# Optimization experiments

Measured on AMD Instinct MI355X. Metric: run time of the kernel, lower is better.

## Reference

```python
import jax, jax.numpy as jnp
import numpy as np

B, C, H, W = 64, 1, 512, 512
THRESHOLD = 50.0
LEVELS = 3


def _haar_dwt2(x):
    """Single-level 2D Haar DWT on [B,H,W] (even H,W). Returns (cA,(cH,cV,cD)).
    Matches pywt 'haar' coefficient magnitudes (sign conventions are irrelevant
    to the loss, which is odd-symmetric through soft-threshold and uses |.|)."""
    a = x[:, 0::2, 0::2]
    b = x[:, 0::2, 1::2]
    c = x[:, 1::2, 0::2]
    d = x[:, 1::2, 1::2]
    half = jnp.float32(0.5)
    cA = (a + b + c + d) * half
    cH = (a + b - c - d) * half  # low along cols, high along rows
    cV = (a - b + c - d) * half  # high along cols, low along rows
    cD = (a - b - c + d) * half  # high/high
    return cA, (cH, cV, cD)


def _wavedec2(x, levels):
    """Multi-level DWT. Returns detail tuples ordered coarsest-first,
    matching pywt.wavedec2 list order coeffs[1:]."""
    details = []
    cA = x
    for _ in range(levels):
        cA, d = _haar_dwt2(cA)
        details.append(d)
    details.reverse()  # coarsest first
    return details


def _soft_threshold(x, thr):
    return jnp.sign(x) * jnp.maximum(jnp.abs(x) - thr, 0.0)


def setup_inputs() -> dict:
    key = jax.random.key(0)
    k1, k2 = jax.random.split(key)
    pred = jax.random.uniform(k1, (B, C, H, W), dtype=jnp.float32)
    target = jax.random.uniform(k2, (B, C, H, W), dtype=jnp.float32)
    return {"pred": pred, "target": target}


def reference(pred, target):
    p = pred[:, 0]   # [B,H,W]
    t = target[:, 0]
    det_p = _wavedec2(p, LEVELS)
    det_t = _wavedec2(t, LEVELS)
    total = jnp.float32(0.0)
    for level_idx in range(1, LEVELS + 1):
        # per-level adaptive threshold, normalized to [0,1] image range
        thr = jnp.float32((THRESHOLD / 2.0 ** (level_idx - 1)) / 255.0)
        level_weight = jnp.float32(1.0 / level_idx)
        dp = det_p[level_idx - 1]
        dt = det_t[level_idx - 1]
        level_loss = jnp.float32(0.0)
        for k in range(3):  # cH, cV, cD
            diff = _soft_threshold(dp[k], thr) - _soft_threshold(dt[k], thr)
            level_loss = level_loss + jnp.mean(jnp.abs(diff))
        total = total + level_weight * level_loss / 3.0
    # per-sample sum / valid_samples == batch mean (all samples valid here)
    return total
```

## Files before the change

kernel.cpp:

```cpp
#include <hip/hip_runtime.h>


#define IMG_H 512
#define IMG_W 512
#define N_BATCH 64

#define THR1 (50.0f / 255.0f)
#define THR2 (25.0f / 255.0f)
#define THR3 (12.5f / 255.0f)

#define GRID_BLOCKS 2048
#define N_ITERS 2

__device__ __forceinline__ float softthr(float x, float thr) {
    float m = fmaxf(fabsf(x) - thr, 0.0f);
    return copysignf(m, x);
}

__device__ __forceinline__ float detail_term(float p, float t, float thr) {
    return fabsf(softthr(p, thr) - softthr(t, thr));
}

__device__ __forceinline__ void haar_quad(float a, float b, float c, float d,
                                          float& cA, float& cH, float& cV, float& cD) {
    cA = 0.5f * (a + b + c + d);
    cH = 0.5f * (a + b - c - d);
    cV = 0.5f * (a - b + c - d);
    cD = 0.5f * (a - b - c + d);
}

__global__ __launch_bounds__(256, 8)
void wavelet_main(const float* __restrict__ pred,
                  const float* __restrict__ target,
                  float* __restrict__ ws) {
    constexpr float W1 = 1.0f / (1.0f * 3.0f * (float)(N_BATCH * 256 * 256));
    constexpr float W2 = 1.0f / (2.0f * 3.0f * (float)(N_BATCH * 128 * 128));
    constexpr float W3 = 1.0f / (3.0f * 3.0f * (float)(N_BATCH * 64 * 64));

    const int tid0 = blockIdx.x * 256 + threadIdx.x;
    float acc = 0.0f;

    #pragma unroll
    for (int iter = 0; iter < N_ITERS; ++iter) {
        const int it   = tid0 + iter * (GRID_BLOCKS * 256);
        const int lane = it & 63;
        const int wv   = it >> 6;
        const int img  = wv >> 8;
        const int ww   = wv & 255;
        const int wcy  = ww >> 2;
        const int wcx  = ww & 3;
        const int half = lane >> 5;
        const int li   = lane & 31;

        const int r0 = 8 * wcy + 4 * half;
        const int c0 = 128 * wcx + 4 * li;
        const long base = (long)img * (IMG_H * IMG_W) + (long)r0 * IMG_W + c0;

        const float4 p0 = *(const float4*)(pred + base);
        const float4 p1 = *(const float4*)(pred + base + IMG_W);
        const float4 p2 = *(const float4*)(pred + base + 2 * IMG_W);
        const float4 p3 = *(const float4*)(pred + base + 3 * IMG_W);
        const float4 t0 = *(const float4*)(target + base);
        const float4 t1 = *(const float4*)(target + base + IMG_W);
        const float4 t2 = *(const float4*)(target + base + 2 * IMG_W);
        const float4 t3 = *(const float4*)(target + base + 3 * IMG_W);

        float s1 = 0.0f;
        float cA1p[4], cA1t[4];
        {
            float cA, cH, cV, cD, cAt, cHt, cVt, cDt;
            haar_quad(p0.x, p0.y, p1.x, p1.y, cA, cH, cV, cD);
            haar_quad(t0.x, t0.y, t1.x, t1.y, cAt, cHt, cVt, cDt);
            s1 += detail_term(cH, cHt, THR1) + detail_term(cV, cVt, THR1) + detail_term(cD, cDt, THR1);
            cA1p[0] = cA; cA1t[0] = cAt;

            haar_quad(p0.z, p0.w, p1.z, p1.w, cA, cH, cV, cD);
            haar_quad(t0.z, t0.w, t1.z, t1.w, cAt, cHt, cVt, cDt);
            s1 += detail_term(cH, cHt, THR1) + detail_term(cV, cVt, THR1) + detail_term(cD, cDt, THR1);
            cA1p[1] = cA; cA1t[1] = cAt;

            haar_quad(p2.x, p2.y, p3.x, p3.y, cA, cH, cV, cD);
            haar_quad(t2.x, t2.y, t3.x, t3.y, cAt, cHt, cVt, cDt);
            s1 += detail_term(cH, cHt, THR1) + detail_term(cV, cVt, THR1) + detail_term(cD, cDt, THR1);
            cA1p[2] = cA; cA1t[2] = cAt;

            haar_quad(p2.z, p2.w, p3.z, p3.w, cA, cH, cV, cD);
            haar_quad(t2.z, t2.w, t3.z, t3.w, cAt, cHt, cVt, cDt);
            s1 += detail_term(cH, cHt, THR1) + detail_term(cV, cVt, THR1) + detail_term(cD, cDt, THR1);
            cA1p[3] = cA; cA1t[3] = cAt;
        }

        float s2 = 0.0f;
        float cA2p, cA2t;
        {
            float cH, cV, cD, cHt, cVt, cDt;
            haar_quad(cA1p[0], cA1p[1], cA1p[2], cA1p[3], cA2p, cH, cV, cD);
            haar_quad(cA1t[0], cA1t[1], cA1t[2], cA1t[3], cA2t, cHt, cVt, cDt);
            s2 = detail_term(cH, cHt, THR2) + detail_term(cV, cVt, THR2) + detail_term(cD, cDt, THR2);
        }

        float s3 = 0.0f;
        {
            float pV = __shfl_xor(cA2p, 32);
            float tV = __shfl_xor(cA2t, 32);
            float pH = __shfl_xor(cA2p, 1);
            float tH = __shfl_xor(cA2t, 1);
            float pD = __shfl_xor(pV, 1);
            float tD = __shfl_xor(tV, 1);
            float cA, cH, cV, cD, cAt, cHt, cVt, cDt;
            haar_quad(cA2p, pH, pV, pD, cA, cH, cV, cD);
            haar_quad(cA2t, tH, tV, tD, cAt, cHt, cVt, cDt);
            s3 = detail_term(cH, cHt, THR3) + detail_term(cV, cVt, THR3) + detail_term(cD, cDt, THR3);
        }
        const float w3 = ((lane & 33) == 0) ? W3 : 0.0f;

        acc += W1 * s1 + W2 * s2 + w3 * s3;
    }

    #pragma unroll
    for (int off = 32; off > 0; off >>= 1)
        acc += __shfl_down(acc, off, 64);

    __shared__ float wave_sums[4];
    const int lane_b = threadIdx.x & 63;
    const int wave_b = threadIdx.x >> 6;
    if (lane_b == 0) wave_sums[wave_b] = acc;
    __syncthreads();
    if (threadIdx.x == 0)
        ws[blockIdx.x] = wave_sums[0] + wave_sums[1] + wave_sums[2] + wave_sums[3];
}

__global__ __launch_bounds__(256)
void wavelet_reduce(const float* __restrict__ ws, float* __restrict__ out) {
    const int tidx = threadIdx.x;
    float v = 0.0f;
    #pragma unroll
    for (int k = 0; k < GRID_BLOCKS / 256; ++k)
        v += ws[tidx + k * 256];

    #pragma unroll
    for (int off = 32; off > 0; off >>= 1)
        v += __shfl_down(v, off, 64);

    __shared__ float wave_sums[4];
    const int lane = tidx & 63;
    const int wave = tidx >> 6;
    if (lane == 0) wave_sums[wave] = v;
    __syncthreads();
    if (tidx == 0)
        out[0] = wave_sums[0] + wave_sums[1] + wave_sums[2] + wave_sums[3];
}

extern "C" void kernel_launch(void* const* d_in, const int* in_sizes, int n_in,
                              void* d_out, int out_size, void* d_ws, size_t ws_size,
                              hipStream_t stream) {
    const float* pred   = (const float*)d_in[0];
    const float* target = (const float*)d_in[1];
    float* out = (float*)d_out;
    float* ws  = (float*)d_ws;

    wavelet_main<<<GRID_BLOCKS, 256, 0, stream>>>(pred, target, ws);
    wavelet_reduce<<<1, 256, 0, stream>>>(ws, out);
}
```

Baseline: 141.4 us.

## Remap waves to 8-row strips with software-pipelined double-buffered loads

After: 143.9 us. No clear change (+1.8%).

```diff
diff --git a/kernel.cpp b/kernel.cpp
--- a/kernel.cpp
+++ b/kernel.cpp
@@ -1,7 +1,6 @@
 #include <hip/hip_runtime.h>
 
 
-#define IMG_H 512
 #define IMG_W 512
 #define N_BATCH 64
 
@@ -9,8 +8,9 @@
 #define THR2 (25.0f / 255.0f)
 #define THR3 (12.5f / 255.0f)
 
-#define GRID_BLOCKS 2048
-#define N_ITERS 2
+#define NBLK 1024
+#define N_WAVES (NBLK * 4)
+#define N_TILES 8192
 
 __device__ __forceinline__ float softthr(float x, float thr) {
     float m = fmaxf(fabsf(x) - thr, 0.0f);
@@ -29,7 +29,9 @@
     cD = 0.5f * (a - b - c + d);
 }
 
-__global__ __launch_bounds__(256, 8)
+__device__ __forceinline__ float4 ld4(const float* p) { return *(const float4*)p; }
+
+__global__ __launch_bounds__(256, 4)
 void wavelet_main(const float* __restrict__ pred,
                   const float* __restrict__ target,
                   float* __restrict__ ws) {
@@ -37,82 +39,80 @@
     constexpr float W2 = 1.0f / (2.0f * 3.0f * (float)(N_BATCH * 128 * 128));
     constexpr float W3 = 1.0f / (3.0f * 3.0f * (float)(N_BATCH * 64 * 64));
 
-    const int tid0 = blockIdx.x * 256 + threadIdx.x;
+    const int wid = blockIdx.x * 4 + (threadIdx.x >> 6);
+    const int li  = threadIdx.x & 63;
+
     float acc = 0.0f;
 
     #pragma unroll
-    for (int iter = 0; iter < N_ITERS; ++iter) {
-        const int it   = tid0 + iter * (GRID_BLOCKS * 256);
-        const int lane = it & 63;
-        const int wv   = it >> 6;
-        const int img  = wv >> 8;
-        const int ww   = wv & 255;
-        const int wcy  = ww >> 2;
-        const int wcx  = ww & 3;
-        const int half = lane >> 5;
-        const int li   = lane & 31;
+    for (int t = 0; t < 2; ++t) {
+        const int T     = wid + t * N_WAVES;
+        const int img   = T >> 7;
+        const int rem   = T & 127;
+        const int half  = rem & 1;
+        const int strip = rem >> 1;
 
-        const int r0 = 8 * wcy + 4 * half;
-        const int c0 = 128 * wcx + 4 * li;
-        const long base = (long)img * (IMG_H * IMG_W) + (long)r0 * IMG_W + c0;
+        const size_t off = (size_t)img * (512 * 512)
+                         + (size_t)strip * 8 * IMG_W
+                         + half * 256 + 4 * li;
+        const float* pb = pred + off;
+        const float* tb = target + off;
 
-        const float4 p0 = *(const float4*)(pred + base);
-        const float4 p1 = *(const float4*)(pred + base + IMG_W);
-        const float4 p2 = *(const float4*)(pred + base + 2 * IMG_W);
-        const float4 p3 = *(const float4*)(pred + base + 3 * IMG_W);
-        const float4 t0 = *(const float4*)(target + base);
-        const float4 t1 = *(const float4*)(target + base + IMG_W);
-        const float4 t2 = *(const float4*)(target + base + 2 * IMG_W);
-        const float4 t3 = *(const float4*)(target + base + 3 * IMG_W);
+        float4 Pa[2], Pb[2], Ta[2], Tb[2];
+        Pa[0] = ld4(pb);            Pb[0] = ld4(pb + IMG_W);
+        Ta[0] = ld4(tb);            Tb[0] = ld4(tb + IMG_W);
+        Pa[1] = ld4(pb + 1024);     Pb[1] = ld4(pb + 1536);
+        Ta[1] = ld4(tb + 1024);     Tb[1] = ld4(tb + 1536);
 
-        float s1 = 0.0f;
-        float cA1p[4], cA1t[4];
-        {
+        float s1 = 0.0f, s2 = 0.0f;
+        float cA1p[4][2], cA1t[4][2];
+
+        #pragma unroll
+        for (int rp = 0; rp < 4; ++rp) {
+            const int bsel = rp & 1;
+            const float4 p0 = Pa[bsel], p1 = Pb[bsel];
+            const float4 q0 = Ta[bsel], q1 = Tb[bsel];
+
+            if (rp < 2) {
+                const int o = (rp + 2) * 1024;
+                Pa[bsel] = ld4(pb + o);         Pb[bsel] = ld4(pb + o + IMG_W);
+                Ta[bsel] = ld4(tb + o);         Tb[bsel] = ld4(tb + o + IMG_W);
+            }
+
             float cA, cH, cV, cD, cAt, cHt, cVt, cDt;
             haar_quad(p0.x, p0.y, p1.x, p1.y, cA, cH, cV, cD);
-            haar_quad(t0.x, t0.y, t1.x, t1.y, cAt, cHt, cVt, cDt);
+            haar_quad(q0.x, q0.y, q1.x, q1.y, cAt, cHt, cVt, cDt);
             s1 += detail_term(cH, cHt, THR1) + detail_term(cV, cVt, THR1) + detail_term(cD, cDt, THR1);
-            cA1p[0] = cA; cA1t[0] = cAt;
-
+            cA1p[rp][0] = cA; cA1t[rp][0] = cAt;
             haar_quad(p0.z, p0.w, p1.z, p1.w, cA, cH, cV, cD);
-            haar_quad(t0.z, t0.w, t1.z, t1.w, cAt, cHt, cVt, cDt);
+            haar_quad(q0.z, q0.w, q1.z, q1.w, cAt, cHt, cVt, cDt);
             s1 += detail_term(cH, cHt, THR1) + detail_term(cV, cVt, THR1) + detail_term(cD, cDt, THR1);
-            cA1p[1] = cA; cA1t[1] = cAt;
-
-            haar_quad(p2.x, p2.y, p3.x, p3.y, cA, cH, cV, cD);
-            haar_quad(t2.x, t2.y, t3.x, t3.y, cAt, cHt, cVt, cDt);
-            s1 += detail_term(cH, cHt, THR1) + detail_term(cV, cVt, THR1) + detail_term(cD, cDt, THR1);
-            cA1p[2] = cA; cA1t[2] = cAt;
-
-            haar_quad(p2.z, p2.w, p3.z, p3.w, cA, cH, cV, cD);
-            haar_quad(t2.z, t2.w, t3.z, t3.w, cAt, cHt, cVt, cDt);
-            s1 += detail_term(cH, cHt, THR1) + detail_term(cV, cVt, THR1) + detail_term(cD, cDt, THR1);
-            cA1p[3] = cA; cA1t[3] = cAt;
+            cA1p[rp][1] = cA; cA1t[rp][1] = cAt;
         }
 
-        float s2 = 0.0f;
-        float cA2p, cA2t;
+        float cA2p[2], cA2t[2];
         {
             float cH, cV, cD, cHt, cVt, cDt;
-            haar_quad(cA1p[0], cA1p[1], cA1p[2], cA1p[3], cA2p, cH, cV, cD);
-            haar_quad(cA1t[0], cA1t[1], cA1t[2], cA1t[3], cA2t, cHt, cVt, cDt);
-            s2 = detail_term(cH, cHt, THR2) + detail_term(cV, cVt, THR2) + detail_term(cD, cDt, THR2);
+            haar_quad(cA1p[0][0], cA1p[0][1], cA1p[1][0], cA1p[1][1], cA2p[0], cH, cV, cD);
+            haar_quad(cA1t[0][0], cA1t[0][1], cA1t[1][0], cA1t[1][1], cA2t[0], cHt, cVt, cDt);
+            s2 += detail_term(cH, cHt, THR2) + detail_term(cV, cVt, THR2) + detail_term(cD, cDt, THR2);
+            haar_quad(cA1p[2][0], cA1p[2][1], cA1p[3][0], cA1p[3][1], cA2p[1], cH, cV, cD);
+            haar_quad(cA1t[2][0], cA1t[2][1], cA1t[3][0], cA1t[3][1], cA2t[1], cHt, cVt, cDt);
+            s2 += detail_term(cH, cHt, THR2) + detail_term(cV, cVt, THR2) + detail_term(cD, cDt, THR2);
         }
 
-        float s3 = 0.0f;
+        float s3;
         {
-            float pV = __shfl_xor(cA2p, 32);
-            float tV = __shfl_xor(cA2t, 32);
-            float pH = __shfl_xor(cA2p, 1);
-            float tH = __shfl_xor(cA2t, 1);
-            float pD = __shfl_xor(pV, 1);
-            float tD = __shfl_xor(tV, 1);
+            const float bP = __shfl_xor(cA2p[0], 1);
+            const float dP = __shfl_xor(cA2p[1], 1);
+            const float bT = __shfl_xor(cA2t[0], 1);
+            const float dT = __shfl_xor(cA2t[1], 1);
             float cA, cH, cV, cD, cAt, cHt, cVt, cDt;
-            haar_quad(cA2p, pH, pV, pD, cA, cH, cV, cD);
-            haar_quad(cA2t, tH, tV, tD, cAt, cHt, cVt, cDt);
+            haar_quad(cA2p[0], bP, cA2p[1], dP, cA, cH, cV, cD);
+            haar_quad(cA2t[0], bT, cA2t[1], dT, cAt, cHt, cVt, cDt);
             s3 = detail_term(cH, cHt, THR3) + detail_term(cV, cVt, THR3) + detail_term(cD, cDt, THR3);
         }
-        const float w3 = ((lane & 33) == 0) ? W3 : 0.0f;
+        const float w3 = (li & 1) ? 0.0f : W3;
 
         acc += W1 * s1 + W2 * s2 + w3 * s3;
     }
@@ -135,7 +135,7 @@
     const int tidx = threadIdx.x;
     float v = 0.0f;
     #pragma unroll
-    for (int k = 0; k < GRID_BLOCKS / 256; ++k)
+    for (int k = 0; k < NBLK / 256; ++k)
         v += ws[tidx + k * 256];
 
     #pragma unroll
@@ -159,6 +159,6 @@
     float* out = (float*)d_out;
     float* ws  = (float*)d_ws;
 
-    wavelet_main<<<GRID_BLOCKS, 256, 0, stream>>>(pred, target, ws);
+    wavelet_main<<<NBLK, 256, 0, stream>>>(pred, target, ws);
     wavelet_reduce<<<1, 256, 0, stream>>>(ws, out);
 }
```

## Double-buffer tiles into LDS via direct global-to-LDS async loads

Applied to the files above, without the earlier changes.

Result: slower. 145.4 us (+2.8%).

```diff
diff --git a/kernel.cpp b/kernel.cpp
--- a/kernel.cpp
+++ b/kernel.cpp
@@ -1,7 +1,6 @@
 #include <hip/hip_runtime.h>
 
 
-#define IMG_H 512
 #define IMG_W 512
 #define N_BATCH 64
 
@@ -9,8 +8,11 @@
 #define THR2 (25.0f / 255.0f)
 #define THR3 (12.5f / 255.0f)
 
-#define GRID_BLOCKS 2048
-#define N_ITERS 2
+#define NBLK 1024
+#define NT   8
+
+typedef __attribute__((address_space(1))) const void* gas_t;
+typedef __attribute__((address_space(3))) void*       las_t;
 
 __device__ __forceinline__ float softthr(float x, float thr) {
     float m = fmaxf(fabsf(x) - thr, 0.0f);
@@ -29,105 +31,117 @@
     cD = 0.5f * (a - b - c + d);
 }
 
-__global__ __launch_bounds__(256, 8)
+__global__ __launch_bounds__(256)
 void wavelet_main(const float* __restrict__ pred,
                   const float* __restrict__ target,
                   float* __restrict__ ws) {
+    __shared__ float lds[2][2][8][256];
+
     constexpr float W1 = 1.0f / (1.0f * 3.0f * (float)(N_BATCH * 256 * 256));
     constexpr float W2 = 1.0f / (2.0f * 3.0f * (float)(N_BATCH * 128 * 128));
     constexpr float W3 = 1.0f / (3.0f * 3.0f * (float)(N_BATCH * 64 * 64));
 
-    const int tid0 = blockIdx.x * 256 + threadIdx.x;
+    const int t = threadIdx.x;
+    const int w = t >> 6;
+    const int l = t & 63;
+
     float acc = 0.0f;
 
-    #pragma unroll
-    for (int iter = 0; iter < N_ITERS; ++iter) {
-        const int it   = tid0 + iter * (GRID_BLOCKS * 256);
-        const int lane = it & 63;
-        const int wv   = it >> 6;
-        const int img  = wv >> 8;
-        const int ww   = wv & 255;
-        const int wcy  = ww >> 2;
-        const int wcx  = ww & 3;
-        const int half = lane >> 5;
-        const int li   = lane & 31;
+    auto stage = [&](int T, int buf) {
+        const int img   = T >> 7;
+        const int rem   = T & 127;
+        const int half  = rem & 1;
+        const int strip = rem >> 1;
+        const size_t base = (size_t)img * (512 * 512)
+                          + (size_t)(strip * 8) * IMG_W
+                          + half * 256 + l * 4;
+        #pragma unroll
+        for (int k = 0; k < 4; ++k) {
+            const int slot = 4 * w + k;
+            const int inp  = slot >> 3;
+            const int row  = slot & 7;
+            const float* g = (inp ? target : pred) + base + (size_t)row * IMG_W;
+            __builtin_amdgcn_global_load_lds((gas_t)(const void*)g,
+                                             (las_t)(void*)&lds[buf][inp][row][0],
+                                             16, 0, 0);
+        }
+    };
 
-        const int r0 = 8 * wcy + 4 * half;
-        const int c0 = 128 * wcx + 4 * li;
-        const long base = (long)img * (IMG_H * IMG_W) + (long)r0 * IMG_W + c0;
+    stage(blockIdx.x, 0);
 
-        const float4 p0 = *(const float4*)(pred + base);
-        const float4 p1 = *(const float4*)(pred + base + IMG_W);
-        const float4 p2 = *(const float4*)(pred + base + 2 * IMG_W);
-        const float4 p3 = *(const float4*)(pred + base + 3 * IMG_W);
-        const float4 t0 = *(const float4*)(target + base);
-        const float4 t1 = *(const float4*)(target + base + IMG_W);
-        const float4 t2 = *(const float4*)(target + base + 2 * IMG_W);
-        const float4 t3 = *(const float4*)(target + base + 3 * IMG_W);
+    for (int it = 0; it < NT; ++it) {
+        const int buf = it & 1;
+        __syncthreads();
+        if (it + 1 < NT) stage(blockIdx.x + (it + 1) * NBLK, buf ^ 1);
 
-        float s1 = 0.0f;
-        float cA1p[4], cA1t[4];
-        {
-            float cA, cH, cV, cD, cAt, cHt, cVt, cDt;
-            haar_quad(p0.x, p0.y, p1.x, p1.y, cA, cH, cV, cD);
-            haar_quad(t0.x, t0.y, t1.x, t1.y, cAt, cHt, cVt, cDt);
-            s1 += detail_term(cH, cHt, THR1) + detail_term(cV, cVt, THR1) + detail_term(cD, cDt, THR1);
-            cA1p[0] = cA; cA1t[0] = cAt;
+        if (w < 2) {
+            const int g4  = l >> 2;
+            const int sub = l & 3;
+            const int br  = sub >> 1;
+            const int bc  = w * 32 + g4 * 2 + (sub & 1);
 
-            haar_quad(p0.z, p0.w, p1.z, p1.w, cA, cH, cV, cD);
-            haar_quad(t0.z, t0.w, t1.z, t1.w, cAt, cHt, cVt, cDt);
-            s1 += detail_term(cH, cHt, THR1) + detail_term(cV, cVt, THR1) + detail_term(cD, cDt, THR1);
-            cA1p[1] = cA; cA1t[1] = cAt;
+            float4 P[4], Q[4];
+            #pragma unroll
+            for (int r = 0; r < 4; ++r) {
+                P[r] = *(const float4*)&lds[buf][0][br * 4 + r][bc * 4];
+                Q[r] = *(const float4*)&lds[buf][1][br * 4 + r][bc * 4];
+            }
 
-            haar_quad(p2.x, p2.y, p3.x, p3.y, cA, cH, cV, cD);
-            haar_quad(t2.x, t2.y, t3.x, t3.y, cAt, cHt, cVt, cDt);
-            s1 += detail_term(cH, cHt, THR1) + detail_term(cV, cVt, THR1) + detail_term(cD, cDt, THR1);
-            cA1p[2] = cA; cA1t[2] = cAt;
+            float s1 = 0.0f;
+            float cA1p[4], cA1t[4];
+            {
+                float cA, cH, cV, cD, cAt, cHt, cVt, cDt;
+                haar_quad(P[0].x, P[0].y, P[1].x, P[1].y, cA, cH, cV, cD);
+                haar_quad(Q[0].x, Q[0].y, Q[1].x, Q[1].y, cAt, cHt, cVt, cDt);
+                s1 += detail_term(cH, cHt, THR1) + detail_term(cV, cVt, THR1) + detail_term(cD, cDt, THR1);
+                cA1p[0] = cA; cA1t[0] = cAt;
 
-            haar_quad(p2.z, p2.w, p3.z, p3.w, cA, cH, cV, cD);
-            haar_quad(t2.z, t2.w, t3.z, t3.w, cAt, cHt, cVt, cDt);
-            s1 += detail_term(cH, cHt, THR1) + detail_term(cV, cVt, THR1) + detail_term(cD, cDt, THR1);
-            cA1p[3] = cA; cA1t[3] = cAt;
+                haar_quad(P[0].z, P[0].w, P[1].z, P[1].w, cA, cH, cV, cD);
+                haar_quad(Q[0].z, Q[0].w, Q[1].z, Q[1].w, cAt, cHt, cVt, cDt);
+                s1 += detail_term(cH, cHt, THR1) + detail_term(cV, cVt, THR1) + detail_term(cD, cDt, THR1);
+                cA1p[1] = cA; cA1t[1] = cAt;
+
+                haar_quad(P[2].x, P[2].y, P[3].x, P[3].y, cA, cH, cV, cD);
+                haar_quad(Q[2].x, Q[2].y, Q[3].x, Q[3].y, cAt, cHt, cVt, cDt);
+                s1 += detail_term(cH, cHt, THR1) + detail_term(cV, cVt, THR1) + detail_term(cD, cDt, THR1);
+                cA1p[2] = cA; cA1t[2] = cAt;
+
+                haar_quad(P[2].z, P[2].w, P[3].z, P[3].w, cA, cH, cV, cD);
+                haar_quad(Q[2].z, Q[2].w, Q[3].z, Q[3].w, cAt, cHt, cVt, cDt);
+                s1 += detail_term(cH, cHt, THR1) + detail_term(cV, cVt, THR1) + detail_term(cD, cDt, THR1);
+                cA1p[3] = cA; cA1t[3] = cAt;
+            }
+
+            float s2, cA2p, cA2t;
+            {
+                float cH, cV, cD, cHt, cVt, cDt;
+                haar_quad(cA1p[0], cA1p[1], cA1p[2], cA1p[3], cA2p, cH, cV, cD);
+                haar_quad(cA1t[0], cA1t[1], cA1t[2], cA1t[3], cA2t, cHt, cVt, cDt);
+                s2 = detail_term(cH, cHt, THR2) + detail_term(cV, cVt, THR2) + detail_term(cD, cDt, THR2);
+            }
+
+            float s3;
+            {
+                float vp[4], vt[4];
+                vp[sub]     = cA2p;                vt[sub]     = cA2t;
+                vp[sub ^ 1] = __shfl_xor(cA2p, 1); vt[sub ^ 1] = __shfl_xor(cA2t, 1);
+                vp[sub ^ 2] = __shfl_xor(cA2p, 2); vt[sub ^ 2] = __shfl_xor(cA2t, 2);
+                vp[sub ^ 3] = __shfl_xor(cA2p, 3); vt[sub ^ 3] = __shfl_xor(cA2t, 3);
+                float cA, cH, cV, cD, cAt, cHt, cVt, cDt;
+                haar_quad(vp[0], vp[1], vp[2], vp[3], cA, cH, cV, cD);
+                haar_quad(vt[0], vt[1], vt[2], vt[3], cAt, cHt, cVt, cDt);
+                s3 = detail_term(cH, cHt, THR3) + detail_term(cV, cVt, THR3) + detail_term(cD, cDt, THR3);
+            }
+            const float w3 = (sub == 0) ? W3 : 0.0f;
+
+            acc += W1 * s1 + W2 * s2 + w3 * s3;
         }
-
-        float s2 = 0.0f;
-        float cA2p, cA2t;
-        {
-            float cH, cV, cD, cHt, cVt, cDt;
-            haar_quad(cA1p[0], cA1p[1], cA1p[2], cA1p[3], cA2p, cH, cV, cD);
-            haar_quad(cA1t[0], cA1t[1], cA1t[2], cA1t[3], cA2t, cHt, cVt, cDt);
-            s2 = detail_term(cH, cHt, THR2) + detail_term(cV, cVt, THR2) + detail_term(cD, cDt, THR2);
-        }
-
-        float s3 = 0.0f;
-        {
-            float pV = __shfl_xor(cA2p, 32);
-            float tV = __shfl_xor(cA2t, 32);
-            float pH = __shfl_xor(cA2p, 1);
-            float tH = __shfl_xor(cA2t, 1);
-            float pD = __shfl_xor(pV, 1);
-            float tD = __shfl_xor(tV, 1);
-            float cA, cH, cV, cD, cAt, cHt, cVt, cDt;
-            haar_quad(cA2p, pH, pV, pD, cA, cH, cV, cD);
-            haar_quad(cA2t, tH, tV, tD, cAt, cHt, cVt, cDt);
-            s3 = detail_term(cH, cHt, THR3) + detail_term(cV, cVt, THR3) + detail_term(cD, cDt, THR3);
-        }
-        const float w3 = ((lane & 33) == 0) ? W3 : 0.0f;
-
-        acc += W1 * s1 + W2 * s2 + w3 * s3;
     }
 
     #pragma unroll
     for (int off = 32; off > 0; off >>= 1)
         acc += __shfl_down(acc, off, 64);
-
-    __shared__ float wave_sums[4];
-    const int lane_b = threadIdx.x & 63;
-    const int wave_b = threadIdx.x >> 6;
-    if (lane_b == 0) wave_sums[wave_b] = acc;
-    __syncthreads();
-    if (threadIdx.x == 0)
-        ws[blockIdx.x] = wave_sums[0] + wave_sums[1] + wave_sums[2] + wave_sums[3];
+    if (l == 0) ws[blockIdx.x * 4 + w] = acc;
 }
 
 __global__ __launch_bounds__(256)
@@ -135,7 +149,7 @@
     const int tidx = threadIdx.x;
     float v = 0.0f;
     #pragma unroll
-    for (int k = 0; k < GRID_BLOCKS / 256; ++k)
+    for (int k = 0; k < (NBLK * 4) / 256; ++k)
         v += ws[tidx + k * 256];
 
     #pragma unroll
@@ -159,6 +173,6 @@
     float* out = (float*)d_out;
     float* ws  = (float*)d_ws;
 
-    wavelet_main<<<GRID_BLOCKS, 256, 0, stream>>>(pred, target, ws);
+    wavelet_main<<<NBLK, 256, 0, stream>>>(pred, target, ws);
     wavelet_reduce<<<1, 256, 0, stream>>>(ws, out);
 }
```
